# Kernel optimization log

Measured on AMD Instinct MI355X. Metric: run time of the kernel, lower is better.

## Reference

```python
import jax, jax.numpy as jnp
import numpy as np
import math

QUERY_LEN = 64
VALUES_LEN = 64
NUM_HEADS = 16


def setup_inputs() -> dict:
    key = jax.random.key(0)
    k1, k2, k3, k4 = jax.random.split(key, 4)
    B, G, N = 2, 4, 1024
    D = QUERY_LEN * NUM_HEADS  # 1024
    queries = jax.random.normal(k1, (B, G, N, D), dtype=jnp.float32)
    keys = jax.random.normal(k2, (B, G, N, D), dtype=jnp.float32)
    values = jax.random.normal(k3, (B, G, N, VALUES_LEN * NUM_HEADS), dtype=jnp.float32)
    neuron_bank_connectivity_sub = jax.random.uniform(k4, (1, G, 1, N, N), dtype=jnp.float32)
    return {
        "queries": queries,
        "keys": keys,
        "values": values,
        "neuron_bank_connectivity_sub": neuron_bank_connectivity_sub,
    }


def reference(queries, keys, values, neuron_bank_connectivity_sub):
    B, G, N, _ = queries.shape
    H, dq, dv = NUM_HEADS, QUERY_LEN, VALUES_LEN
    # view last dim as (vec_len, num_heads), move heads forward: [B,G,H,N,d]
    q = queries.reshape(B, G, N, dq, H).transpose(0, 1, 4, 2, 3)
    k = keys.reshape(B, G, N, dq, H).transpose(0, 1, 4, 2, 3)
    v = values.reshape(B, G, N, dv, H).transpose(0, 1, 4, 2, 3)
    scores = jnp.einsum('bghnd,bghmd->bghnm', q, k) / math.sqrt(dq)
    probs = jax.nn.softmax(scores - neuron_bank_connectivity_sub, axis=-1)
    out = jnp.einsum('bghnm,bghmd->bghnd', probs, v)  # [B,G,H,N,dv]
    # Faithful to original: view() applied to the contiguous [B,G,H,N,dv] buffer
    return out.reshape(B, G, N, H * dv)
```

## Files before the change

### kernel.cpp

```cpp
#include <hip/hip_runtime.h>
#include <hip/hip_bf16.h>
#include <math.h>

#define B_ 2
#define G_ 4
#define N_ 1024
#define H_ 16
#define D_ 64
#define BG_ (B_*G_)
#define BGH_ (B_*G_*H_)
#define MK 64
#define LOG2E 1.44269504f
#define QSCALE (0.125f * LOG2E)

typedef __bf16 bf16;
typedef bf16 bf16x8 __attribute__((ext_vector_type(8)));
typedef bf16 bf16x2 __attribute__((ext_vector_type(2)));
typedef float f32x4 __attribute__((ext_vector_type(4)));
typedef float f32x16 __attribute__((ext_vector_type(16)));
typedef int i32x4 __attribute__((ext_vector_type(4)));
typedef unsigned u32x2 __attribute__((ext_vector_type(2)));

static __device__ __forceinline__ f32x16 mfma32(bf16x8 a, bf16x8 b, f32x16 c) {
    return __builtin_amdgcn_mfma_f32_32x32x16_bf16(a, b, c, 0, 0, 0);
}

static __device__ __forceinline__ unsigned pk2(float a, float b) {
    bf16x2 t; t[0] = (bf16)a; t[1] = (bf16)b;
    return __builtin_bit_cast(unsigned, t);
}

static __device__ __forceinline__ void pl32swap(unsigned& a, unsigned& b, int hi) {
#if __has_builtin(__builtin_amdgcn_permlane32_swap)
    u32x2 r = __builtin_amdgcn_permlane32_swap(a, b, false, false);
    a = r[0]; b = r[1];
    (void)hi;
#else
    unsigned ax = (unsigned)__shfl_xor((int)a, 32, 64);
    unsigned bx = (unsigned)__shfl_xor((int)b, 32, 64);
    unsigned na = hi ? bx : a;
    unsigned nb = hi ? b : ax;
    a = na; b = nb;
#endif
}

#define HS 1160
#define NS 72

__global__ __launch_bounds__(256) void transpose_fused(
    const float* __restrict__ q, const float* __restrict__ k, const float* __restrict__ v,
    bf16* __restrict__ qt, bf16* __restrict__ ktb, bf16* __restrict__ vtT)
{
    __shared__ __attribute__((aligned(16))) bf16 lds[16 * HS];
    int bx = blockIdx.x;
    int tensor = bx >> 9;
    int rr = bx & 511;
    int bg = rr >> 6;
    int tile = rr & 63;
    int n0 = tile * 16;
    int t = threadIdx.x;

    const float* src = (tensor == 0) ? q : (tensor == 1) ? k : v;
    float scale = (tensor == 0) ? QSCALE : 1.0f;
    const float* sb = src + (size_t)bg * N_ * 1024 + (size_t)n0 * 1024;

    int h0 = 4 * (t & 3);
    int d  = t >> 2;
    int wbase = h0 * HS + d;
#pragma unroll 4
    for (int i = 0; i < 16; ++i) {
        float4 val = ((const float4*)(sb + (size_t)i * 1024))[t];
        bf16* p = &lds[wbase + i * NS];
        p[0]        = (bf16)(val.x * scale);
        p[HS]       = (bf16)(val.y * scale);
        p[2 * HS]   = (bf16)(val.z * scale);
        p[3 * HS]   = (bf16)(val.w * scale);
    }
    __syncthreads();

    if (tensor < 2) {
        bf16* dst = (tensor == 0) ? qt : ktb;
        int n  = (t >> 3) & 15;
        int db = t & 7;
        int hb = t >> 7;
#pragma unroll
        for (int i = 0; i < 8; ++i) {
            int h = 2 * i + hb;
            bf16x8 vv = *(const bf16x8*)(&lds[h * HS + n * NS + db * 8]);
            *(bf16x8*)(dst + (((size_t)(bg * H_ + h)) * N_ + n0 + n) * D_ + db * 8) = vv;
        }
    } else {
        int dd = t & 63;
        int nc = (t >> 6) & 1;
        int hb = t >> 7;
#pragma unroll
        for (int i = 0; i < 8; ++i) {
            int h = 2 * i + hb;
            bf16x8 vv;
#pragma unroll
            for (int jj = 0; jj < 8; ++jj)
                vv[jj] = lds[h * HS + (nc * 8 + jj) * NS + dd];
            *(bf16x8*)(vtT + (((size_t)(bg * H_ + h)) * D_ + dd) * N_ + n0 + nc * 8) = vv;
        }
    }
}

__global__ __launch_bounds__(256, 2) void flash_kernel(
    const bf16* __restrict__ qt, const bf16* __restrict__ kt, const bf16* __restrict__ vtT,
    const float* __restrict__ bias, float* __restrict__ out)
{
    __shared__ __attribute__((aligned(16))) bf16 k_lds[2][MK][72];
    __shared__ __attribute__((aligned(16))) bf16 v_lds[2][D_][72];
    __shared__ __attribute__((aligned(16))) float bias_lds[4][32][68];

    int tid  = threadIdx.x;
    int w    = tid >> 6;
    int lane = tid & 63;
    int hi   = lane >> 5;
    int q31  = lane & 31;
    int key  = (q31 & 3) << 4;

    int bgh = blockIdx.y;
    int n0  = blockIdx.x * 128;
    int g   = (bgh >> 4) & (G_ - 1);

    const bf16* qb_base = qt + ((size_t)bgh * N_ + n0 + w * 32 + q31) * D_ + hi * 8;
    bf16x8 qb[4];
#pragma unroll
    for (int c = 0; c < 4; ++c) qb[c] = *(const bf16x8*)(qb_base + c * 16);

    f32x16 acc0 = {0,0,0,0,0,0,0,0,0,0,0,0,0,0,0,0};
    f32x16 acc1 = {0,0,0,0,0,0,0,0,0,0,0,0,0,0,0,0};
    float l = 0.f;

    int srow = tid >> 2;
    int j    = tid & 3;
    int jsw  = (j ^ (srow & 3)) * 16;
    const bf16* kp = kt + (size_t)bgh * N_ * D_ + (size_t)srow * D_ + j * 16;
    const bf16* vp = vtT + ((size_t)bgh * D_ + srow) * N_ + j * 16;

    int brow = lane >> 1;
    int bh2  = lane & 1;
    const float* bbL = bias + (size_t)g * N_ * N_ + (size_t)(n0 + w * 32 + brow) * N_ + bh2 * 32;

    bf16x8 kr0 = *(const bf16x8*)(kp);
    bf16x8 kr1 = *(const bf16x8*)(kp + 8);
    bf16x8 vr0 = *(const bf16x8*)(vp);
    bf16x8 vr1 = *(const bf16x8*)(vp + 8);
    f32x4 bnx[8];
#pragma unroll
    for (int kk = 0; kk < 8; ++kk) bnx[kk] = *(const f32x4*)(bbL + kk * 4);

    *(bf16x8*)(&k_lds[0][srow][jsw])     = kr0;
    *(bf16x8*)(&k_lds[0][srow][jsw + 8]) = kr1;
    *(bf16x8*)(&v_lds[0][srow][jsw])     = vr0;
    *(bf16x8*)(&v_lds[0][srow][jsw + 8]) = vr1;
#pragma unroll
    for (int kk = 0; kk < 8; ++kk) {
        int pos = ((bh2 * 8 + kk) + 2 * brow) & 15;
        *(f32x4*)(&bias_lds[w][brow][pos * 4]) = bnx[kk];
    }

    for (int it = 0; it < N_ / MK; ++it) {
        int  cur  = it & 1;
        bool more = (it + 1 < N_ / MK);
        __syncthreads();

        if (more) {
            kp += MK * D_;  vp += MK;
            kr0 = *(const bf16x8*)(kp);
            kr1 = *(const bf16x8*)(kp + 8);
            vr0 = *(const bf16x8*)(vp);
            vr1 = *(const bf16x8*)(vp + 8);
#pragma unroll
            for (int kk = 0; kk < 8; ++kk)
                bnx[kk] = *(const f32x4*)(bbL + (it + 1) * MK + kk * 4);
        }

        f32x4 bv[2][4];
#pragma unroll
        for (int t = 0; t < 2; ++t)
#pragma unroll
            for (int u = 0; u < 4; ++u) {
                int pos = ((t * 8 + 2 * u + hi) + 2 * q31) & 15;
                bv[t][u] = *(const f32x4*)(&bias_lds[w][q31][pos * 4]);
            }

        f32x16 s0 = {0,0,0,0,0,0,0,0,0,0,0,0,0,0,0,0};
        f32x16 s1 = {0,0,0,0,0,0,0,0,0,0,0,0,0,0,0,0};
        __builtin_amdgcn_s_setprio(1);
#pragma unroll
        for (int c = 0; c < 4; ++c) {
            bf16x8 kb0 = *(const bf16x8*)(&k_lds[cur][q31]     [((c << 4) ^ key) + hi * 8]);
            bf16x8 kb1 = *(const bf16x8*)(&k_lds[cur][32 + q31][((c << 4) ^ key) + hi * 8]);
            s0 = mfma32(kb0, qb[c], s0);
            s1 = mfma32(kb1, qb[c], s1);
        }
        __builtin_amdgcn_s_setprio(0);

        unsigned wa[2][4], wb[2][4];
#pragma unroll
        for (int t = 0; t < 2; ++t) {
#pragma unroll
            for (int u = 0; u < 4; ++u) {
                const f32x16& s = t ? s1 : s0;
                float p0 = __builtin_amdgcn_exp2f(__builtin_fmaf(-LOG2E, bv[t][u][0], s[4*u+0]));
                float p1 = __builtin_amdgcn_exp2f(__builtin_fmaf(-LOG2E, bv[t][u][1], s[4*u+1]));
                float p2 = __builtin_amdgcn_exp2f(__builtin_fmaf(-LOG2E, bv[t][u][2], s[4*u+2]));
                float p3 = __builtin_amdgcn_exp2f(__builtin_fmaf(-LOG2E, bv[t][u][3], s[4*u+3]));
                l += (p0 + p1) + (p2 + p3);
                wa[t][u] = pk2(p0, p1);
                wb[t][u] = pk2(p2, p3);
            }
        }

        if (more) {
#pragma unroll
            for (int kk = 0; kk < 8; ++kk) {
                int pos = ((bh2 * 8 + kk) + 2 * brow) & 15;
                *(f32x4*)(&bias_lds[w][brow][pos * 4]) = bnx[kk];
            }
        }

#pragma unroll
        for (int t = 0; t < 2; ++t) {
            pl32swap(wa[t][0], wa[t][1], hi);
            pl32swap(wb[t][0], wb[t][1], hi);
            pl32swap(wa[t][2], wa[t][3], hi);
            pl32swap(wb[t][2], wb[t][3], hi);
        }

        __builtin_amdgcn_s_setprio(1);
#pragma unroll
        for (int t = 0; t < 2; ++t)
#pragma unroll
            for (int c01 = 0; c01 < 2; ++c01) {
                int kc = t * 2 + c01;
                i32x4 bwi = { (int)wa[t][2*c01], (int)wb[t][2*c01],
                              (int)wa[t][2*c01+1], (int)wb[t][2*c01+1] };
                bf16x8 pb = __builtin_bit_cast(bf16x8, bwi);
                bf16x8 va0 = *(const bf16x8*)(&v_lds[cur][q31]     [((kc << 4) ^ key) + hi * 8]);
                bf16x8 va1 = *(const bf16x8*)(&v_lds[cur][32 + q31][((kc << 4) ^ key) + hi * 8]);
                acc0 = mfma32(va0, pb, acc0);
                acc1 = mfma32(va1, pb, acc1);
            }
        __builtin_amdgcn_s_setprio(0);

        if (more) {
            int nxt = cur ^ 1;
            *(bf16x8*)(&k_lds[nxt][srow][jsw])     = kr0;
            *(bf16x8*)(&k_lds[nxt][srow][jsw + 8]) = kr1;
            *(bf16x8*)(&v_lds[nxt][srow][jsw])     = vr0;
            *(bf16x8*)(&v_lds[nxt][srow][jsw + 8]) = vr1;
        }
    }

    l += __shfl_xor(l, 32, 64);
    float inv = 1.0f / l;

    float* ob = out + ((size_t)bgh * N_ + n0 + w * 32 + q31) * D_ + hi * 4;
#pragma unroll
    for (int td = 0; td < 2; ++td) {
        const f32x16& a = td ? acc1 : acc0;
#pragma unroll
        for (int u = 0; u < 4; ++u) {
            f32x4 o = { a[4*u+0] * inv, a[4*u+1] * inv, a[4*u+2] * inv, a[4*u+3] * inv };
            *(f32x4*)(ob + td * 32 + u * 8) = o;
        }
    }
}

__global__ __launch_bounds__(256) void naive_kernel(
    const float* __restrict__ q, const float* __restrict__ k,
    const float* __restrict__ v, const float* __restrict__ bias,
    float* __restrict__ out)
{
    __shared__ float sc[N_];
    __shared__ float red[256];
    __shared__ float qrow[64];
    int n = blockIdx.x;
    int bgh = blockIdx.y;
    int bg = bgh >> 4, h = bgh & 15;
    int g = bg & (G_ - 1);
    int tid = threadIdx.x;
    const float* qr = q + ((size_t)(bg * N_ + n)) * 1024;
    if (tid < 64) qrow[tid] = qr[tid * 16 + h];
    __syncthreads();
    const float* bb = bias + (size_t)g * N_ * N_ + (size_t)n * N_;
    for (int m = tid; m < N_; m += 256) {
        const float* kr = k + ((size_t)(bg * N_ + m)) * 1024 + h;
        float dot = 0.f;
        for (int d = 0; d < 64; ++d) dot += qrow[d] * kr[d * 16];
        sc[m] = dot * 0.125f - bb[m];
    }
    __syncthreads();
    float mx = -INFINITY;
    for (int m = tid; m < N_; m += 256) mx = fmaxf(mx, sc[m]);
    red[tid] = mx; __syncthreads();
    for (int s = 128; s > 0; s >>= 1) {
        if (tid < s) red[tid] = fmaxf(red[tid], red[tid + s]);
        __syncthreads();
    }
    float M = red[0]; __syncthreads();
    float sum = 0.f;
    for (int m = tid; m < N_; m += 256) { float e = __expf(sc[m] - M); sc[m] = e; sum += e; }
    red[tid] = sum; __syncthreads();
    for (int s = 128; s > 0; s >>= 1) {
        if (tid < s) red[tid] += red[tid + s];
        __syncthreads();
    }
    float L = red[0]; __syncthreads();
    int d = tid & 63, quarter = tid >> 6;
    float acc = 0.f;
    const float* vb = v + (size_t)bg * N_ * 1024 + d * 16 + h;
    for (int m = quarter * 256; m < quarter * 256 + 256; ++m) acc += sc[m] * vb[(size_t)m * 1024];
    red[tid] = acc; __syncthreads();
    if (tid < 64) {
        float o = (red[tid] + red[tid + 64] + red[tid + 128] + red[tid + 192]) / L;
        out[((size_t)bgh * N_ + n) * 64 + d] = o;
    }
}

extern "C" void kernel_launch(void* const* d_in, const int* in_sizes, int n_in,
                              void* d_out, int out_size, void* d_ws, size_t ws_size,
                              hipStream_t stream) {
    const float* q    = (const float*)d_in[0];
    const float* k    = (const float*)d_in[1];
    const float* v    = (const float*)d_in[2];
    const float* bias = (const float*)d_in[3];
    float* out = (float*)d_out;

    const size_t elems = (size_t)BGH_ * N_ * D_;
    const size_t need  = 3 * elems * sizeof(bf16);

    if (ws_size >= need) {
        bf16* qt  = (bf16*)d_ws;
        bf16* ktb = qt + elems;
        bf16* vtT = ktb + elems;
        transpose_fused<<<3 * 512, 256, 0, stream>>>(q, k, v, qt, ktb, vtT);
        dim3 grid(N_ / 128, BGH_);
        flash_kernel<<<grid, 256, 0, stream>>>(qt, ktb, vtT, bias, out);
    } else {
        dim3 grid(N_, BGH_);
        naive_kernel<<<grid, 256, 0, stream>>>(q, k, v, bias, out);
    }
}
```

Before: 237.1 us.

## Load K/V tiles via direct global-to-LDS and pre-permute bias layout

The flash kernel now loads K and V tiles with global_load_lds straight into LDS, split so two waves load K and two load V, with an XOR swizzle and no register staging. V is rewritten by the transpose pass into 16-key chunked blocks. A new prepass permutes the bias into an MFMA-fragment-friendly layout so each lane reads it directly from global into registers, dropping the bias LDS buffer. Occupancy is raised to 3 blocks per SM. The cost is an extra full-bias copy in the workspace and a larger prepass, and the path now needs a bigger workspace, falling back to the naive kernel if it is too small.

Measured after the change: 213.7 us. 1.11x faster.

```diff
diff --git a/kernel.cpp b/kernel.cpp
--- a/kernel.cpp
+++ b/kernel.cpp
@@ -44,21 +44,60 @@
 #endif
 }
 
+static __device__ __forceinline__ void gll16(const void* gsrc, void* ldst, int lane) {
+#if __has_builtin(__builtin_amdgcn_global_load_lds)
+    (void)lane;
+    __builtin_amdgcn_global_load_lds((const __attribute__((address_space(1))) void*)gsrc,
+                                     (__attribute__((address_space(3))) void*)ldst, 16, 0, 0);
+#else
+    *(bf16x8*)((bf16*)ldst + lane * 8) = *(const bf16x8*)((const bf16*)gsrc);
+#endif
+}
+
 #define HS 1160
 #define NS 72
 
 __global__ __launch_bounds__(256) void transpose_fused(
     const float* __restrict__ q, const float* __restrict__ k, const float* __restrict__ v,
-    bf16* __restrict__ qt, bf16* __restrict__ ktb, bf16* __restrict__ vtT)
+    const float* __restrict__ bias,
+    bf16* __restrict__ qt, bf16* __restrict__ ktb, bf16* __restrict__ vtT16,
+    float* __restrict__ biasX)
 {
     __shared__ __attribute__((aligned(16))) bf16 lds[16 * HS];
     int bx = blockIdx.x;
+    int t = threadIdx.x;
+
+    if (bx >= 3 * 512) {
+        int idx = bx - 3 * 512;
+        int gg  = idx >> 8;
+        int tl  = idx & 255;
+        int q0  = (tl >> 4) * 64;
+        int m0  = (tl & 15) * 64;
+        float* ldsF = (float*)lds;
+
+        int mi = t & 15, qr = t >> 4;
+#pragma unroll
+        for (int rr = 0; rr < 4; ++rr) {
+            int row = qr + rr * 16;
+            f32x4 val = *(const f32x4*)(bias + ((size_t)(gg * N_ + q0 + row) * N_ + m0 + 4 * mi));
+            *(f32x4*)(&ldsF[row * 68 + 4 * mi]) = val;
+        }
+        __syncthreads();
+        int qr2 = t & 63, mb0 = t >> 6;
+#pragma unroll
+        for (int kk = 0; kk < 4; ++kk) {
+            int mbi = mb0 + kk * 4;
+            f32x4 vv = *(const f32x4*)(&ldsF[qr2 * 68 + 4 * mbi]);
+            *(f32x4*)(biasX + (((size_t)gg * 256 + m0 / 4 + mbi) * N_ + q0 + qr2) * 4) = vv;
+        }
+        return;
+    }
+
     int tensor = bx >> 9;
     int rr = bx & 511;
     int bg = rr >> 6;
     int tile = rr & 63;
     int n0 = tile * 16;
-    int t = threadIdx.x;
 
     const float* src = (tensor == 0) ? q : (tensor == 1) ? k : v;
     float scale = (tensor == 0) ? QSCALE : 1.0f;
@@ -91,34 +130,36 @@
         }
     } else {
         int dd = t & 63;
-        int nc = (t >> 6) & 1;
-        int hb = t >> 7;
-#pragma unroll
-        for (int i = 0; i < 8; ++i) {
-            int h = 2 * i + hb;
-            bf16x8 vv;
-#pragma unroll
-            for (int jj = 0; jj < 8; ++jj)
-                vv[jj] = lds[h * HS + (nc * 8 + jj) * NS + dd];
-            *(bf16x8*)(vtT + (((size_t)(bg * H_ + h)) * D_ + dd) * N_ + n0 + nc * 8) = vv;
-        }
-    }
-}
-
-__global__ __launch_bounds__(256, 2) void flash_kernel(
-    const bf16* __restrict__ qt, const bf16* __restrict__ kt, const bf16* __restrict__ vtT,
-    const float* __restrict__ bias, float* __restrict__ out)
+        int hb = t >> 6;
+#pragma unroll
+        for (int i = 0; i < 4; ++i) {
+            int h = hb * 4 + i;
+            bf16x8 v0, v1;
+#pragma unroll
+            for (int jj = 0; jj < 8; ++jj) v0[jj] = lds[h * HS + jj * NS + dd];
+#pragma unroll
+            for (int jj = 0; jj < 8; ++jj) v1[jj] = lds[h * HS + (8 + jj) * NS + dd];
+            bf16* dst = vtT16 + (((size_t)(bg * H_ + h) * 64 + tile) * D_ + dd) * 16;
+            *(bf16x8*)dst       = v0;
+            *(bf16x8*)(dst + 8) = v1;
+        }
+    }
+}
+
+__global__ __launch_bounds__(256, 3) void flash_kernel(
+    const bf16* __restrict__ qt, const bf16* __restrict__ kt, const bf16* __restrict__ vtT16,
+    const float* __restrict__ biasX, float* __restrict__ out)
 {
-    __shared__ __attribute__((aligned(16))) bf16 k_lds[2][MK][72];
-    __shared__ __attribute__((aligned(16))) bf16 v_lds[2][D_][72];
-    __shared__ __attribute__((aligned(16))) float bias_lds[4][32][68];
+    __shared__ __attribute__((aligned(16))) bf16 k_lds[2][MK][D_];
+    __shared__ __attribute__((aligned(16))) bf16 v_lds[2][D_][MK];
 
     int tid  = threadIdx.x;
     int w    = tid >> 6;
     int lane = tid & 63;
     int hi   = lane >> 5;
     int q31  = lane & 31;
-    int key  = (q31 & 3) << 4;
+    int key8 = (q31 & 7) << 3;
+    int hi8  = hi << 3;
 
     int bgh = blockIdx.y;
     int n0  = blockIdx.x * 128;
@@ -133,33 +174,29 @@
     f32x16 acc1 = {0,0,0,0,0,0,0,0,0,0,0,0,0,0,0,0};
     float l = 0.f;
 
-    int srow = tid >> 2;
-    int j    = tid & 3;
-    int jsw  = (j ^ (srow & 3)) * 16;
-    const bf16* kp = kt + (size_t)bgh * N_ * D_ + (size_t)srow * D_ + j * 16;
-    const bf16* vp = vtT + ((size_t)bgh * D_ + srow) * N_ + j * 16;
-
-    int brow = lane >> 1;
-    int bh2  = lane & 1;
-    const float* bbL = bias + (size_t)g * N_ * N_ + (size_t)(n0 + w * 32 + brow) * N_ + bh2 * 32;
-
-    bf16x8 kr0 = *(const bf16x8*)(kp);
-    bf16x8 kr1 = *(const bf16x8*)(kp + 8);
-    bf16x8 vr0 = *(const bf16x8*)(vp);
-    bf16x8 vr1 = *(const bf16x8*)(vp + 8);
+    int rloc = lane >> 3;
+    int c16  = lane & 7;
+    int csw  = c16 ^ rloc;
+    bool isK = (w < 2);
+    int wrow = (w & 1) * 32;
+    const bf16* ksrc = kt + (size_t)bgh * N_ * D_ + (size_t)(wrow + rloc) * D_ + csw * 8;
+    const bf16* vsrc = vtT16 + (((size_t)bgh * 64 + (csw >> 1)) * D_ + (wrow + rloc)) * 16 + (csw & 1) * 8;
+
+    const float* bb = biasX + (size_t)g * (256u * 1024 * 4) + (size_t)(n0 + w * 32 + q31) * 4;
+
+    if (isK) {
+#pragma unroll
+        for (int i = 0; i < 4; ++i) gll16(ksrc + (size_t)i * 8 * D_, &k_lds[0][wrow + i * 8][0], lane);
+    } else {
+#pragma unroll
+        for (int i = 0; i < 4; ++i) gll16(vsrc + (size_t)i * 128, &v_lds[0][wrow + i * 8][0], lane);
+    }
     f32x4 bnx[8];
 #pragma unroll
-    for (int kk = 0; kk < 8; ++kk) bnx[kk] = *(const f32x4*)(bbL + kk * 4);
-
-    *(bf16x8*)(&k_lds[0][srow][jsw])     = kr0;
-    *(bf16x8*)(&k_lds[0][srow][jsw + 8]) = kr1;
-    *(bf16x8*)(&v_lds[0][srow][jsw])     = vr0;
-    *(bf16x8*)(&v_lds[0][srow][jsw + 8]) = vr1;
-#pragma unroll
-    for (int kk = 0; kk < 8; ++kk) {
-        int pos = ((bh2 * 8 + kk) + 2 * brow) & 15;
-        *(f32x4*)(&bias_lds[w][brow][pos * 4]) = bnx[kk];
-    }
+    for (int tt = 0; tt < 2; ++tt)
+#pragma unroll
+        for (int u = 0; u < 4; ++u)
+            bnx[tt * 4 + u] = *(const f32x4*)(bb + (size_t)(tt * 8 + 2 * u + hi) * 4096);
 
     for (int it = 0; it < N_ / MK; ++it) {
         int  cur  = it & 1;
@@ -167,32 +204,26 @@
         __syncthreads();
 
         if (more) {
-            kp += MK * D_;  vp += MK;
-            kr0 = *(const bf16x8*)(kp);
-            kr1 = *(const bf16x8*)(kp + 8);
-            vr0 = *(const bf16x8*)(vp);
-            vr1 = *(const bf16x8*)(vp + 8);
-#pragma unroll
-            for (int kk = 0; kk < 8; ++kk)
-                bnx[kk] = *(const f32x4*)(bbL + (it + 1) * MK + kk * 4);
-        }
-
-        f32x4 bv[2][4];
-#pragma unroll
-        for (int t = 0; t < 2; ++t)
-#pragma unroll
-            for (int u = 0; u < 4; ++u) {
-                int pos = ((t * 8 + 2 * u + hi) + 2 * q31) & 15;
-                bv[t][u] = *(const f32x4*)(&bias_lds[w][q31][pos * 4]);
+            int nxt = cur ^ 1;
+            if (isK) {
+                const bf16* ks = ksrc + (size_t)(it + 1) * MK * D_;
+#pragma unroll
+                for (int i = 0; i < 4; ++i) gll16(ks + (size_t)i * 8 * D_, &k_lds[nxt][wrow + i * 8][0], lane);
+            } else {
+                const bf16* vs = vsrc + (size_t)(it + 1) * 4096;
+#pragma unroll
+                for (int i = 0; i < 4; ++i) gll16(vs + (size_t)i * 128, &v_lds[nxt][wrow + i * 8][0], lane);
             }
+        }
 
         f32x16 s0 = {0,0,0,0,0,0,0,0,0,0,0,0,0,0,0,0};
         f32x16 s1 = {0,0,0,0,0,0,0,0,0,0,0,0,0,0,0,0};
         __builtin_amdgcn_s_setprio(1);
 #pragma unroll
         for (int c = 0; c < 4; ++c) {
-            bf16x8 kb0 = *(const bf16x8*)(&k_lds[cur][q31]     [((c << 4) ^ key) + hi * 8]);
-            bf16x8 kb1 = *(const bf16x8*)(&k_lds[cur][32 + q31][((c << 4) ^ key) + hi * 8]);
+            int off = ((c << 4) | hi8) ^ key8;
+            bf16x8 kb0 = *(const bf16x8*)(&k_lds[cur][q31][off]);
+            bf16x8 kb1 = *(const bf16x8*)(&k_lds[cur][32 + q31][off]);
             s0 = mfma32(kb0, qb[c], s0);
             s1 = mfma32(kb1, qb[c], s1);
         }
@@ -200,59 +231,53 @@
 
         unsigned wa[2][4], wb[2][4];
 #pragma unroll
-        for (int t = 0; t < 2; ++t) {
+        for (int tt = 0; tt < 2; ++tt) {
 #pragma unroll
             for (int u = 0; u < 4; ++u) {
-                const f32x16& s = t ? s1 : s0;
-                float p0 = __builtin_amdgcn_exp2f(__builtin_fmaf(-LOG2E, bv[t][u][0], s[4*u+0]));
-                float p1 = __builtin_amdgcn_exp2f(__builtin_fmaf(-LOG2E, bv[t][u][1], s[4*u+1]));
-                float p2 = __builtin_amdgcn_exp2f(__builtin_fmaf(-LOG2E, bv[t][u][2], s[4*u+2]));
-                float p3 = __builtin_amdgcn_exp2f(__builtin_fmaf(-LOG2E, bv[t][u][3], s[4*u+3]));
+                const f32x16& s = tt ? s1 : s0;
+                f32x4 bvv = bnx[tt * 4 + u];
+                float p0 = __builtin_amdgcn_exp2f(__builtin_fmaf(-LOG2E, bvv[0], s[4*u+0]));
+                float p1 = __builtin_amdgcn_exp2f(__builtin_fmaf(-LOG2E, bvv[1], s[4*u+1]));
+                float p2 = __builtin_amdgcn_exp2f(__builtin_fmaf(-LOG2E, bvv[2], s[4*u+2]));
+                float p3 = __builtin_amdgcn_exp2f(__builtin_fmaf(-LOG2E, bvv[3], s[4*u+3]));
                 l += (p0 + p1) + (p2 + p3);
-                wa[t][u] = pk2(p0, p1);
-                wb[t][u] = pk2(p2, p3);
+                wa[tt][u] = pk2(p0, p1);
+                wb[tt][u] = pk2(p2, p3);
             }
         }
 
         if (more) {
 #pragma unroll
-            for (int kk = 0; kk < 8; ++kk) {
-                int pos = ((bh2 * 8 + kk) + 2 * brow) & 15;
-                *(f32x4*)(&bias_lds[w][brow][pos * 4]) = bnx[kk];
-            }
-        }
-
-#pragma unroll
-        for (int t = 0; t < 2; ++t) {
-            pl32swap(wa[t][0], wa[t][1], hi);
-            pl32swap(wb[t][0], wb[t][1], hi);
-            pl32swap(wa[t][2], wa[t][3], hi);
-            pl32swap(wb[t][2], wb[t][3], hi);
+            for (int tt = 0; tt < 2; ++tt)
+#pragma unroll
+                for (int u = 0; u < 4; ++u)
+                    bnx[tt * 4 + u] = *(const f32x4*)(bb + (size_t)((it + 1) * 16 + tt * 8 + 2 * u + hi) * 4096);
+        }
+
+#pragma unroll
+        for (int tt = 0; tt < 2; ++tt) {
+            pl32swap(wa[tt][0], wa[tt][1], hi);
+            pl32swap(wb[tt][0], wb[tt][1], hi);
+            pl32swap(wa[tt][2], wa[tt][3], hi);
+            pl32swap(wb[tt][2], wb[tt][3], hi);
         }
 
         __builtin_amdgcn_s_setprio(1);
 #pragma unroll
-        for (int t = 0; t < 2; ++t)
+        for (int tt = 0; tt < 2; ++tt)
 #pragma unroll
             for (int c01 = 0; c01 < 2; ++c01) {
-                int kc = t * 2 + c01;
-                i32x4 bwi = { (int)wa[t][2*c01], (int)wb[t][2*c01],
-                              (int)wa[t][2*c01+1], (int)wb[t][2*c01+1] };
+                int kc = tt * 2 + c01;
+                i32x4 bwi = { (int)wa[tt][2*c01], (int)wb[tt][2*c01],
+                              (int)wa[tt][2*c01+1], (int)wb[tt][2*c01+1] };
                 bf16x8 pb = __builtin_bit_cast(bf16x8, bwi);
-                bf16x8 va0 = *(const bf16x8*)(&v_lds[cur][q31]     [((kc << 4) ^ key) + hi * 8]);
-                bf16x8 va1 = *(const bf16x8*)(&v_lds[cur][32 + q31][((kc << 4) ^ key) + hi * 8]);
+                int off = ((kc << 4) | hi8) ^ key8;
+                bf16x8 va0 = *(const bf16x8*)(&v_lds[cur][q31][off]);
+                bf16x8 va1 = *(const bf16x8*)(&v_lds[cur][32 + q31][off]);
                 acc0 = mfma32(va0, pb, acc0);
                 acc1 = mfma32(va1, pb, acc1);
             }
         __builtin_amdgcn_s_setprio(0);
-
-        if (more) {
-            int nxt = cur ^ 1;
-            *(bf16x8*)(&k_lds[nxt][srow][jsw])     = kr0;
-            *(bf16x8*)(&k_lds[nxt][srow][jsw + 8]) = kr1;
-            *(bf16x8*)(&v_lds[nxt][srow][jsw])     = vr0;
-            *(bf16x8*)(&v_lds[nxt][srow][jsw + 8]) = vr1;
-        }
     }
 
     l += __shfl_xor(l, 32, 64);
@@ -331,15 +356,17 @@
     float* out = (float*)d_out;
 
     const size_t elems = (size_t)BGH_ * N_ * D_;
-    const size_t need  = 3 * elems * sizeof(bf16);
+    const size_t needA = 3 * elems * sizeof(bf16);
+    const size_t need  = needA + (size_t)G_ * N_ * N_ * 4;
 
     if (ws_size >= need) {
-        bf16* qt  = (bf16*)d_ws;
-        bf16* ktb = qt + elems;
-        bf16* vtT = ktb + elems;
-        transpose_fused<<<3 * 512, 256, 0, stream>>>(q, k, v, qt, ktb, vtT);
+        bf16* qt    = (bf16*)d_ws;
+        bf16* ktb   = qt + elems;
+        bf16* vtT16 = ktb + elems;
+        float* biasX = (float*)((char*)d_ws + needA);
+        transpose_fused<<<3 * 512 + 1024, 256, 0, stream>>>(q, k, v, bias, qt, ktb, vtT16, biasX);
         dim3 grid(N_ / 128, BGH_);
-        flash_kernel<<<grid, 256, 0, stream>>>(qt, ktb, vtT, bias, out);
+        flash_kernel<<<grid, 256, 0, stream>>>(qt, ktb, vtT16, biasX, out);
     } else {
         dim3 grid(N_, BGH_);
         naive_kernel<<<grid, 256, 0, stream>>>(q, k, v, bias, out);
```
